# Performance work log

Hardware: AMD Instinct MI355X
Metric: run time of the kernel (lower is better)

Reference implementation:

```python
import jax, jax.numpy as jnp
import numpy as np

HIDDEN = 4096
N_HEADS = 32
N_KV_HEADS = 8
HEAD_DIM = 128
ROPE_THETA = 10000.0


def setup_inputs() -> dict:
    key = jax.random.key(0)
    ks = jax.random.split(key, 6)
    B, S = 1, 2048
    hidden_states = jax.random.normal(ks[0], (B, S, HIDDEN), dtype=jnp.float32)
    position_ids = jnp.arange(S, dtype=jnp.int64 if jax.config.jax_enable_x64 else jnp.int32)[None, :].astype(jnp.int32)
    scale = 0.02
    Wq = jax.random.normal(ks[1], (HIDDEN, N_HEADS * HEAD_DIM), dtype=jnp.float32) * scale
    Wk = jax.random.normal(ks[2], (HIDDEN, N_KV_HEADS * HEAD_DIM), dtype=jnp.float32) * scale
    Wv = jax.random.normal(ks[3], (HIDDEN, N_KV_HEADS * HEAD_DIM), dtype=jnp.float32) * scale
    Wo = jax.random.normal(ks[4], (N_HEADS * HEAD_DIM, HIDDEN), dtype=jnp.float32) * scale
    return {"hidden_states": hidden_states, "position_ids": position_ids,
            "Wq": Wq, "Wk": Wk, "Wv": Wv, "Wo": Wo}


def _rope_cos_sin(position_ids):
    # neox-style rope over full head_dim (rotary_dim == head_dim)
    half = HEAD_DIM // 2
    inv_freq = 1.0 / (ROPE_THETA ** (jnp.arange(0, half, dtype=jnp.float32) / half))
    angles = position_ids.astype(jnp.float32)[..., None] * inv_freq  # [B, S, half]
    return jnp.cos(angles), jnp.sin(angles)


def _apply_rope(x, cos, sin):
    # x: [B, S, H, D]; cos/sin: [B, S, D/2] broadcast over heads
    x1, x2 = jnp.split(x, 2, axis=-1)
    c = cos[:, :, None, :]
    s = sin[:, :, None, :]
    return jnp.concatenate([x1 * c - x2 * s, x2 * c + x1 * s], axis=-1)


def reference(hidden_states, position_ids, Wq, Wk, Wv, Wo):
    B, S, _ = hidden_states.shape
    q = hidden_states @ Wq  # [B, S, H*D]
    k = hidden_states @ Wk  # [B, S, Hkv*D]
    v = hidden_states @ Wv
    q = q.reshape(B, S, N_HEADS, HEAD_DIM)
    k = k.reshape(B, S, N_KV_HEADS, HEAD_DIM)
    v = v.reshape(B, S, N_KV_HEADS, HEAD_DIM)
    cos, sin = _rope_cos_sin(position_ids)
    q = _apply_rope(q, cos, sin)
    k = _apply_rope(k, cos, sin)
    # GQA: expand kv heads to match query heads
    rep = N_HEADS // N_KV_HEADS
    k = jnp.repeat(k, rep, axis=2)  # [B, S, H, D]
    v = jnp.repeat(v, rep, axis=2)
    scale = 1.0 / jnp.sqrt(jnp.asarray(HEAD_DIM, dtype=q.dtype))
    scores = jnp.einsum('bqhd,bkhd->bhqk', q, k) * scale  # [B, H, S, S]
    causal = jnp.tril(jnp.ones((S, S), dtype=bool))
    scores = jnp.where(causal[None, None], scores, jnp.asarray(-1e30, dtype=scores.dtype))
    probs = jax.nn.softmax(scores, axis=-1)
    attn = jnp.einsum('bhqk,bkhd->bqhd', probs, v)  # [B, S, H, D]
    attn = attn.reshape(B, S, N_HEADS * HEAD_DIM)
    return attn @ Wo  # [B, S, HIDDEN]
```

## Files before the change

kernel.cpp:

```cpp
#include <hip/hip_runtime.h>
#include <hip/hip_bf16.h>
#include <math.h>

#define HIDDEN 4096
#define NH 32
#define NKV 8
#define HD 128
#define QKVC 6144

using f32x4  = __attribute__((ext_vector_type(4))) float;
using frag_ab = __attribute__((ext_vector_type(8))) short;

__device__ __forceinline__ short f2bf(float x){
  __hip_bfloat16 h = __float2bfloat16(x);
  return *reinterpret_cast<short*>(&h);
}
__device__ __forceinline__ float bf2f(short s){
  __hip_bfloat16 h = *reinterpret_cast<__hip_bfloat16*>(&s);
  return __bfloat162float(h);
}

__device__ __forceinline__ void load_lds16(const void* g, void* l){
  __builtin_amdgcn_global_load_lds(
      (const __attribute__((address_space(1))) unsigned*)g,
      (__attribute__((address_space(3))) unsigned*)l, 16, 0, 0);
}

__device__ __forceinline__ void hard_barrier(){
  asm volatile("" ::: "memory");
  __builtin_amdgcn_s_barrier();
  asm volatile("" ::: "memory");
}

__global__ __launch_bounds__(256) void k_cvt(const float* __restrict__ X, short* __restrict__ Y, int n4){
  int i = blockIdx.x*256 + threadIdx.x;
  if (i >= n4) return;
  float4 v = reinterpret_cast<const float4*>(X)[i];
  short4 o;
  o.x = f2bf(v.x); o.y = f2bf(v.y); o.z = f2bf(v.z); o.w = f2bf(v.w);
  reinterpret_cast<short4*>(Y)[i] = o;
}

__global__ __launch_bounds__(256) void k_transpose(const float* __restrict__ W, short* __restrict__ WT,
                                                   int K, int N){
  __shared__ float tile[32][33];
  int n0 = blockIdx.x*32, k0 = blockIdx.y*32;
  int tx = threadIdx.x & 31, ty = threadIdx.x >> 5;
  #pragma unroll
  for (int i=0;i<4;i++) tile[ty+i*8][tx] = W[(size_t)(k0+ty+i*8)*N + n0+tx];
  __syncthreads();
  #pragma unroll
  for (int i=0;i<4;i++) WT[(size_t)(n0+ty+i*8)*K + k0+tx] = f2bf(tile[tx][ty+i*8]);
}

__global__ __launch_bounds__(256) void k_transpose_v(const short* __restrict__ QKV, short* __restrict__ VT){
  __shared__ short tile[32][40];
  int s0 = blockIdx.x*32, d0 = blockIdx.y*32;
  int tx = threadIdx.x & 31, ty = threadIdx.x >> 5;
  #pragma unroll
  for (int i=0;i<4;i++) tile[ty+i*8][tx] = QKV[(size_t)(s0+ty+i*8)*QKVC + 5120 + d0+tx];
  __syncthreads();
  #pragma unroll
  for (int i=0;i<4;i++) VT[(size_t)(d0+ty+i*8)*2048 + s0+tx] = tile[tx][ty+i*8];
}

template<typename OutT>
__global__ __launch_bounds__(512, 4) void k_gemm256(const short* __restrict__ A, const short* __restrict__ BT,
                                                    OutT* __restrict__ C, int M, int N, int K, int mt){
  __shared__ __align__(16) short L[36864];
  const int nwg = gridDim.x, cpx = nwg >> 3;
  const int bid = blockIdx.x;
  const int swz = (bid & 7) * cpx + (bid >> 3);
  const int bx = swz % mt, by = swz / mt;
  const int brow = bx*256, bcol = by*128;
  const int tid = threadIdx.x, lane = tid & 63, wid = tid >> 6;
  const int wr = wid >> 1, wc = wid & 1;
  const int l15 = lane & 15, lg = lane >> 4;
  const int nk = K >> 5;

  const int sr0 = tid >> 2;
  const int scw = ((tid & 3) ^ ((tid >> 3) & 3)) << 3;
  const short* Aponly = A + (size_t)brow*K;
  const short* Bponly = BT + (size_t)bcol*K;

  f32x4 acc[4][4] = {};

  #define STAGE(kt, bb) do { \
    load_lds16(Aponly + (size_t)sr0*K       + (kt)*32 + scw, &L[(bb)*12288 + tid*8]); \
    load_lds16(Aponly + (size_t)(sr0+128)*K + (kt)*32 + scw, &L[(bb)*12288 + (tid+512)*8]); \
    load_lds16(Bponly + (size_t)sr0*K       + (kt)*32 + scw, &L[(bb)*12288 + 8192 + tid*8]); \
  } while(0)

  STAGE(0, 0); STAGE(1, 1);
  asm volatile("s_waitcnt vmcnt(3)" ::: "memory");
  hard_barrier();

  const int rchunk = ((lg ^ ((l15 >> 1) & 3)) << 3);

  int bt = 0;
  for (int t = 0; t < nk; ++t){
    const short* Ab = &L[bt*12288];
    const short* Bb = &L[bt*12288 + 8192];
    frag_ab af[4], bf[4];
    #pragma unroll
    for (int m=0;m<4;m++) af[m] = *(const frag_ab*)&Ab[(wr*64 + m*16 + l15)*32 + rchunk];
    #pragma unroll
    for (int n=0;n<4;n++) bf[n] = *(const frag_ab*)&Bb[(wc*64 + n*16 + l15)*32 + rchunk];
    if (t + 2 < nk){
      int bs = bt + 2; if (bs >= 3) bs -= 3;
      STAGE(t+2, bs);
    }
    __builtin_amdgcn_s_setprio(1);
    #pragma unroll
    for (int m=0;m<4;m++)
      #pragma unroll
      for (int n=0;n<4;n++)
        acc[m][n] = __builtin_amdgcn_mfma_f32_16x16x32_bf16(af[m], bf[n], acc[m][n], 0, 0, 0);
    __builtin_amdgcn_s_setprio(0);
    if (t < nk-2) asm volatile("s_waitcnt vmcnt(3)" ::: "memory");
    else          asm volatile("s_waitcnt vmcnt(0)" ::: "memory");
    hard_barrier();
    bt = (bt == 2) ? 0 : bt + 1;
  }
  #undef STAGE

  #pragma unroll
  for (int m=0;m<4;m++)
    #pragma unroll
    for (int n=0;n<4;n++)
      #pragma unroll
      for (int r=0;r<4;r++){
        size_t row = brow + wr*64 + m*16 + lg*4 + r;
        size_t col = bcol + wc*64 + n*16 + l15;
        float v = acc[m][n][r];
        if constexpr (sizeof(OutT) == 4) C[row*(size_t)N + col] = v;
        else                             C[row*(size_t)N + col] = f2bf(v);
      }
}

__global__ __launch_bounds__(256) void k_rope(short* __restrict__ QKV, const int* __restrict__ pos){
  int idx = blockIdx.x*256 + threadIdx.x;
  int j   = idx & 63;
  int hh  = (idx >> 6) % 40;
  int row = (idx >> 6) / 40;
  int colbase = hh < NH ? hh*HD : HIDDEN + (hh-NH)*HD;
  size_t base = (size_t)row*QKVC + colbase;
  float x1 = bf2f(QKV[base + j]), x2 = bf2f(QKV[base + j + 64]);
  float ang = (float)pos[row] * exp2f(-(float)j * 0.2076205059304601f);
  float sn, cs; sincosf(ang, &sn, &cs);
  QKV[base + j]      = f2bf(x1*cs - x2*sn);
  QKV[base + j + 64] = f2bf(x2*cs + x1*sn);
}

__global__ __launch_bounds__(256) void k_attn(const short* __restrict__ QKV, const short* __restrict__ VT,
                                              short* __restrict__ Attn){
  const int pairI = blockIdx.x, h = blockIdx.y, kvh = h >> 2;
  const int t = threadIdx.x, lane = t & 63, w = t >> 6;
  const int l15 = lane & 15, lg = lane >> 4;
  __shared__ __align__(16) short Ks[32*128];
  __shared__ __align__(16) short Vs[128*40];
  __shared__ __align__(16) short Ps[4][16*40];

  const float SC = 0.08838834764831845f;

  for (int half = 0; half < 2; ++half){
    const int qt = half ? (31 - pairI) : pairI;
    frag_ab aq[4];
    {
      const short* qrow = QKV + (size_t)(qt*64 + w*16 + l15)*QKVC + h*HD;
      #pragma unroll
      for (int ks=0;ks<4;ks++) aq[ks] = *(const frag_ab*)&qrow[ks*32 + lg*8];
    }
    float mrow[4], lrow[4];
    #pragma unroll
    for (int r=0;r<4;r++){ mrow[r] = -INFINITY; lrow[r] = 0.f; }
    f32x4 o[8] = {};
    const int nkv = 2*qt + 2;
    for (int kt = 0; kt < nkv; ++kt){
      __syncthreads();
      #pragma unroll
      for (int i=0;i<2;i++){
        int s = t + i*256;
        int row = s >> 4;
        int c8  = (s & 15) << 3;
        int csw = c8 ^ ((row & 7) << 3);
        load_lds16(QKV + (size_t)(kt*32 + row)*QKVC + HIDDEN + kvh*HD + csw, &Ks[s*8]);
      }
      #pragma unroll
      for (int i=0;i<2;i++){
        int s = t + i*256;
        int d  = s >> 2;
        int k8 = (s & 3) << 3;
        uint4 vv = *(const uint4*)&VT[(size_t)(kvh*HD + d)*2048 + kt*32 + k8];
        *(uint4*)&Vs[d*40 + k8] = vv;
      }
      __syncthreads();
      f32x4 sc[2] = {};
      #pragma unroll
      for (int ks=0;ks<4;ks++){
        int c = ks*32 + lg*8;
        frag_ab b0 = *(const frag_ab*)&Ks[l15*128      + (c ^ ((l15 & 7) << 3))];
        frag_ab b1 = *(const frag_ab*)&Ks[(16+l15)*128 + (c ^ ((l15 & 7) << 3))];
        sc[0] = __builtin_amdgcn_mfma_f32_16x16x32_bf16(aq[ks], b0, sc[0], 0, 0, 0);
        sc[1] = __builtin_amdgcn_mfma_f32_16x16x32_bf16(aq[ks], b1, sc[1], 0, 0, 0);
      }
      float p0[4], p1[4];
      #pragma unroll
      for (int r=0;r<4;r++){
        int rowg = qt*64 + w*16 + lg*4 + r;
        int c0 = kt*32 + l15, c1 = c0 + 16;
        float v0 = sc[0][r]*SC, v1 = sc[1][r]*SC;
        if (c0 > rowg) v0 = -1e30f;
        if (c1 > rowg) v1 = -1e30f;
        float pm = fmaxf(v0, v1);
        pm = fmaxf(pm, __shfl_xor(pm, 1));
        pm = fmaxf(pm, __shfl_xor(pm, 2));
        pm = fmaxf(pm, __shfl_xor(pm, 4));
        pm = fmaxf(pm, __shfl_xor(pm, 8));
        float mn = fmaxf(mrow[r], pm);
        float f  = __expf(mrow[r] - mn);
        mrow[r] = mn;
        float e0 = __expf(v0 - mn), e1 = __expf(v1 - mn);
        float ps = e0 + e1;
        ps += __shfl_xor(ps, 1); ps += __shfl_xor(ps, 2);
        ps += __shfl_xor(ps, 4); ps += __shfl_xor(ps, 8);
        lrow[r] = lrow[r]*f + ps;
        p0[r] = e0; p1[r] = e1;
        #pragma unroll
        for (int df=0;df<8;df++) o[df][r] *= f;
      }
      #pragma unroll
      for (int r=0;r<4;r++){
        Ps[w][(lg*4+r)*40 + l15]      = f2bf(p0[r]);
        Ps[w][(lg*4+r)*40 + 16 + l15] = f2bf(p1[r]);
      }
      frag_ab pa = *(const frag_ab*)&Ps[w][l15*40 + lg*8];
      #pragma unroll
      for (int df=0;df<8;df++){
        frag_ab vb = *(const frag_ab*)&Vs[(df*16+l15)*40 + lg*8];
        o[df] = __builtin_amdgcn_mfma_f32_16x16x32_bf16(pa, vb, o[df], 0, 0, 0);
      }
    }
    #pragma unroll
    for (int df=0;df<8;df++)
      #pragma unroll
      for (int r=0;r<4;r++){
        size_t row = qt*64 + w*16 + lg*4 + r;
        size_t col = (size_t)h*HD + df*16 + l15;
        Attn[row*HIDDEN + col] = f2bf(o[df][r] / lrow[r]);
      }
  }
}

extern "C" void kernel_launch(void* const* d_in, const int* in_sizes, int n_in,
                              void* d_out, int out_size, void* d_ws, size_t ws_size,
                              hipStream_t stream) {
  const float* H  = (const float*)d_in[0];
  const int*  pos = (const int*)  d_in[1];
  const float* Wq = (const float*)d_in[2];
  const float* Wk = (const float*)d_in[3];
  const float* Wv = (const float*)d_in[4];
  const float* Wo = (const float*)d_in[5];
  float* out = (float*)d_out;

  char* ws = (char*)d_ws;
  short* WT   = (short*)(ws);
  short* WoT  = (short*)(ws + 50331648);
  short* Hb   = (short*)(ws + 83886080);
  short* QKV  = (short*)(ws + 100663296);
  short* Attn = (short*)(ws + 125829120);
  short* VT   = Hb;

  k_cvt<<<8192, 256, 0, stream>>>(H, Hb, 2097152);
  k_transpose<<<dim3(128,128), 256, 0, stream>>>(Wq, WT,                        4096, 4096);
  k_transpose<<<dim3( 32,128), 256, 0, stream>>>(Wk, WT + (size_t)4096*4096,    4096, 1024);
  k_transpose<<<dim3( 32,128), 256, 0, stream>>>(Wv, WT + (size_t)5120*4096,    4096, 1024);
  k_transpose<<<dim3(128,128), 256, 0, stream>>>(Wo, WoT,                       4096, 4096);

  k_gemm256<short><<<384, 512, 0, stream>>>(Hb, WT, QKV, 2048, 6144, 4096, 8);
  k_rope<<<20480, 256, 0, stream>>>(QKV, pos);
  k_transpose_v<<<dim3(64,32), 256, 0, stream>>>(QKV, VT);
  k_attn<<<dim3(16,32), 256, 0, stream>>>(QKV, VT, Attn);
  k_gemm256<float><<<256, 512, 0, stream>>>(Attn, WoT, out, 2048, 4096, 4096, 8);
}
```

Measured before the change: 560.2 us.

## Double-buffer K/V tiles with async LDS loads and transposed MFMA softmax layout

Rewrites the attention inner loop to double-buffer K and V tiles in shared memory. V is now loaded asynchronously straight into LDS with an XOR swizzle instead of through registers, and the loads for tile kt+2 are issued while tile kt is computed. The MFMA operands are swapped so each lane holds one query row, which turns the softmax row max/sum into two cross-lane shuffles instead of four per row and lets P and the output be written as packed short4 stores. It also adds s_setprio around the MFMA blocks, at the cost of more LDS and hand-written waitcnt and barrier logic that must stay correct.

Result: faster. 511.0 us (-8.8%).

```diff
diff --git a/kernel.cpp b/kernel.cpp
--- a/kernel.cpp
+++ b/kernel.cpp
@@ -152,103 +152,125 @@
   QKV[base + j + 64] = f2bf(x2*cs + x1*sn);
 }
 
+__device__ __forceinline__ void astage(const short* __restrict__ QKV, const short* __restrict__ VT,
+                                       short* KsB, short* VsB, int kt, int tid, int kvh){
+  #pragma unroll
+  for (int i=0;i<2;i++){
+    int s = tid + i*256;
+    int r = s >> 4, c = (s & 15) << 3;
+    load_lds16(QKV + (size_t)(kt*32 + r)*QKVC + HIDDEN + kvh*HD + (c ^ ((r & 7) << 3)), &KsB[s*8]);
+  }
+  #pragma unroll
+  for (int i=0;i<2;i++){
+    int s = tid + i*256;
+    int r = s >> 2, cw = ((s & 3) ^ ((s >> 3) & 3)) << 3;
+    load_lds16(VT + (size_t)(kvh*HD + r)*2048 + kt*32 + cw, &VsB[s*8]);
+  }
+}
+
 __global__ __launch_bounds__(256) void k_attn(const short* __restrict__ QKV, const short* __restrict__ VT,
                                               short* __restrict__ Attn){
   const int pairI = blockIdx.x, h = blockIdx.y, kvh = h >> 2;
-  const int t = threadIdx.x, lane = t & 63, w = t >> 6;
+  const int tid = threadIdx.x, lane = tid & 63, w = tid >> 6;
   const int l15 = lane & 15, lg = lane >> 4;
-  __shared__ __align__(16) short Ks[32*128];
-  __shared__ __align__(16) short Vs[128*40];
+  __shared__ __align__(16) short Ks[2][32*128];
+  __shared__ __align__(16) short Vs[2][128*32];
   __shared__ __align__(16) short Ps[4][16*40];
 
   const float SC = 0.08838834764831845f;
+  const int vchunk = ((l15 >> 1) & 3);
 
   for (int half = 0; half < 2; ++half){
     const int qt = half ? (31 - pairI) : pairI;
+    const int q_abs = qt*64 + w*16 + l15;
     frag_ab aq[4];
     {
-      const short* qrow = QKV + (size_t)(qt*64 + w*16 + l15)*QKVC + h*HD;
+      const short* qrow = QKV + (size_t)q_abs*QKVC + h*HD;
       #pragma unroll
       for (int ks=0;ks<4;ks++) aq[ks] = *(const frag_ab*)&qrow[ks*32 + lg*8];
     }
-    float mrow[4], lrow[4];
-    #pragma unroll
-    for (int r=0;r<4;r++){ mrow[r] = -INFINITY; lrow[r] = 0.f; }
+    float m = -INFINITY, l = 0.f;
     f32x4 o[8] = {};
     const int nkv = 2*qt + 2;
+
+    astage(QKV, VT, Ks[0], Vs[0], 0, tid, kvh);
+    astage(QKV, VT, Ks[1], Vs[1], 1, tid, kvh);
+    asm volatile("s_waitcnt vmcnt(4)" ::: "memory");
+    hard_barrier();
+
+    int bt = 0;
     for (int kt = 0; kt < nkv; ++kt){
-      __syncthreads();
-      #pragma unroll
-      for (int i=0;i<2;i++){
-        int s = t + i*256;
-        int row = s >> 4;
-        int c8  = (s & 15) << 3;
-        int csw = c8 ^ ((row & 7) << 3);
-        load_lds16(QKV + (size_t)(kt*32 + row)*QKVC + HIDDEN + kvh*HD + csw, &Ks[s*8]);
-      }
-      #pragma unroll
-      for (int i=0;i<2;i++){
-        int s = t + i*256;
-        int d  = s >> 2;
-        int k8 = (s & 3) << 3;
-        uint4 vv = *(const uint4*)&VT[(size_t)(kvh*HD + d)*2048 + kt*32 + k8];
-        *(uint4*)&Vs[d*40 + k8] = vv;
-      }
-      __syncthreads();
-      f32x4 sc[2] = {};
+      f32x4 st[2] = {};
+      __builtin_amdgcn_s_setprio(1);
       #pragma unroll
       for (int ks=0;ks<4;ks++){
         int c = ks*32 + lg*8;
-        frag_ab b0 = *(const frag_ab*)&Ks[l15*128      + (c ^ ((l15 & 7) << 3))];
-        frag_ab b1 = *(const frag_ab*)&Ks[(16+l15)*128 + (c ^ ((l15 & 7) << 3))];
-        sc[0] = __builtin_amdgcn_mfma_f32_16x16x32_bf16(aq[ks], b0, sc[0], 0, 0, 0);
-        sc[1] = __builtin_amdgcn_mfma_f32_16x16x32_bf16(aq[ks], b1, sc[1], 0, 0, 0);
-      }
-      float p0[4], p1[4];
+        frag_ab b0 = *(const frag_ab*)&Ks[bt][l15*128      + (c ^ ((l15 & 7) << 3))];
+        frag_ab b1 = *(const frag_ab*)&Ks[bt][(16+l15)*128 + (c ^ ((l15 & 7) << 3))];
+        st[0] = __builtin_amdgcn_mfma_f32_16x16x32_bf16(b0, aq[ks], st[0], 0, 0, 0);
+        st[1] = __builtin_amdgcn_mfma_f32_16x16x32_bf16(b1, aq[ks], st[1], 0, 0, 0);
+      }
+      __builtin_amdgcn_s_setprio(0);
+      const int kb = kt*32 + lg*4;
+      float v0[4], v1[4];
       #pragma unroll
       for (int r=0;r<4;r++){
-        int rowg = qt*64 + w*16 + lg*4 + r;
-        int c0 = kt*32 + l15, c1 = c0 + 16;
-        float v0 = sc[0][r]*SC, v1 = sc[1][r]*SC;
-        if (c0 > rowg) v0 = -1e30f;
-        if (c1 > rowg) v1 = -1e30f;
-        float pm = fmaxf(v0, v1);
-        pm = fmaxf(pm, __shfl_xor(pm, 1));
-        pm = fmaxf(pm, __shfl_xor(pm, 2));
-        pm = fmaxf(pm, __shfl_xor(pm, 4));
-        pm = fmaxf(pm, __shfl_xor(pm, 8));
-        float mn = fmaxf(mrow[r], pm);
-        float f  = __expf(mrow[r] - mn);
-        mrow[r] = mn;
-        float e0 = __expf(v0 - mn), e1 = __expf(v1 - mn);
-        float ps = e0 + e1;
-        ps += __shfl_xor(ps, 1); ps += __shfl_xor(ps, 2);
-        ps += __shfl_xor(ps, 4); ps += __shfl_xor(ps, 8);
-        lrow[r] = lrow[r]*f + ps;
-        p0[r] = e0; p1[r] = e1;
+        v0[r] = (kb + r      > q_abs) ? -1e30f : st[0][r];
+        v1[r] = (kb + 16 + r > q_abs) ? -1e30f : st[1][r];
+      }
+      float M = fmaxf(fmaxf(fmaxf(v0[0],v0[1]),fmaxf(v0[2],v0[3])),
+                      fmaxf(fmaxf(v1[0],v1[1]),fmaxf(v1[2],v1[3])));
+      M = fmaxf(M, __shfl_xor(M, 16));
+      M = fmaxf(M, __shfl_xor(M, 32));
+      float mn = fmaxf(m, M*SC);
+      float f  = __expf(m - mn);
+      float p0[4], p1[4], ps = 0.f;
+      #pragma unroll
+      for (int r=0;r<4;r++){
+        p0[r] = __expf(fmaf(v0[r], SC, -mn));
+        p1[r] = __expf(fmaf(v1[r], SC, -mn));
+        ps += p0[r] + p1[r];
+      }
+      ps += __shfl_xor(ps, 16);
+      ps += __shfl_xor(ps, 32);
+      l = l*f + ps;
+      m = mn;
+      #pragma unroll
+      for (int df=0;df<8;df++)
         #pragma unroll
-        for (int df=0;df<8;df++) o[df][r] *= f;
-      }
-      #pragma unroll
-      for (int r=0;r<4;r++){
-        Ps[w][(lg*4+r)*40 + l15]      = f2bf(p0[r]);
-        Ps[w][(lg*4+r)*40 + 16 + l15] = f2bf(p1[r]);
-      }
+        for (int r=0;r<4;r++) o[df][r] *= f;
+      short4 w0, w1;
+      w0.x=f2bf(p0[0]); w0.y=f2bf(p0[1]); w0.z=f2bf(p0[2]); w0.w=f2bf(p0[3]);
+      w1.x=f2bf(p1[0]); w1.y=f2bf(p1[1]); w1.z=f2bf(p1[2]); w1.w=f2bf(p1[3]);
+      *(short4*)&Ps[w][l15*40 + lg*4]      = w0;
+      *(short4*)&Ps[w][l15*40 + 16 + lg*4] = w1;
       frag_ab pa = *(const frag_ab*)&Ps[w][l15*40 + lg*8];
+      __builtin_amdgcn_s_setprio(1);
       #pragma unroll
       for (int df=0;df<8;df++){
-        frag_ab vb = *(const frag_ab*)&Vs[(df*16+l15)*40 + lg*8];
-        o[df] = __builtin_amdgcn_mfma_f32_16x16x32_bf16(pa, vb, o[df], 0, 0, 0);
-      }
+        frag_ab vb = *(const frag_ab*)&Vs[bt][(df*16+l15)*32 + ((lg ^ vchunk) << 3)];
+        o[df] = __builtin_amdgcn_mfma_f32_16x16x32_bf16(vb, pa, o[df], 0, 0, 0);
+      }
+      __builtin_amdgcn_s_setprio(0);
+      hard_barrier();
+      if (kt + 2 < nkv){
+        astage(QKV, VT, Ks[bt], Vs[bt], kt+2, tid, kvh);
+        asm volatile("s_waitcnt vmcnt(4)" ::: "memory");
+        hard_barrier();
+      } else if (kt + 1 < nkv){
+        asm volatile("s_waitcnt vmcnt(0)" ::: "memory");
+        hard_barrier();
+      }
+      bt ^= 1;
     }
-    #pragma unroll
-    for (int df=0;df<8;df++)
-      #pragma unroll
-      for (int r=0;r<4;r++){
-        size_t row = qt*64 + w*16 + lg*4 + r;
-        size_t col = (size_t)h*HD + df*16 + l15;
-        Attn[row*HIDDEN + col] = f2bf(o[df][r] / lrow[r]);
-      }
+    float inv = 1.0f / l;
+    #pragma unroll
+    for (int df=0;df<8;df++){
+      short4 s4;
+      s4.x = f2bf(o[df][0]*inv); s4.y = f2bf(o[df][1]*inv);
+      s4.z = f2bf(o[df][2]*inv); s4.w = f2bf(o[df][3]*inv);
+      *(short4*)&Attn[(size_t)q_abs*HIDDEN + h*HD + df*16 + lg*4] = s4;
+    }
   }
 }
 
```
